# Kernel tuning notes

Measured on AMD Instinct MI355X. Metric: run time of the kernel, lower is better.

The kernel has to match this reference:

```python
import jax, jax.numpy as jnp
import numpy as np

SLOPE = 25.0          # snntorch surrogate.fast_sigmoid default slope
ALPHA = 0.05          # attenuation_alpha

@jax.custom_vjp
def spike_fn(x):
    return (x > 0).astype(x.dtype)

def _spike_fwd(x):
    return (x > 0).astype(x.dtype), x

def _spike_bwd(x, g):
    return (g / (SLOPE * jnp.abs(x) + 1.0) ** 2,)

spike_fn.defvjp(_spike_fwd, _spike_bwd)

def lstm_cell(x, h, c, W_ih, W_hh, b_ih, b_hh):
    gates = x @ W_ih.T + b_ih + h @ W_hh.T + b_hh  # [B, 4H]
    i, f, g, o = jnp.split(gates, 4, axis=-1)
    i = jax.nn.sigmoid(i); f = jax.nn.sigmoid(f)
    g = jnp.tanh(g);       o = jax.nn.sigmoid(o)
    c_new = f * c + i * g
    h_new = o * jnp.tanh(c_new)
    return h_new, c_new

def slstm_step(x, syn, mem, W_ih, W_hh, b_ih, b_hh, thr):
    # reset is detached in snntorch (mem_reset -> .detach())
    reset = jax.lax.stop_gradient((mem > thr).astype(mem.dtype))
    h, c = lstm_cell(x, mem, syn, W_ih, W_hh, b_ih, b_hh)
    mem_new = h - reset * thr          # subtract reset mechanism
    spk = spike_fn(mem_new - thr)      # surrogate-gradient spike
    return spk, c, mem_new

def setup_inputs() -> dict:
    key = jax.random.key(0)
    ks = jax.random.split(key, 12)
    T, B, I, H, C = 512, 256, 14, 512, 8
    s = 0.05
    return {
        "x":     jax.random.normal(ks[0], (T, B, I), jnp.float32),
        "W_ih1": jax.random.normal(ks[1], (4 * H, I), jnp.float32) * s,
        "W_hh1": jax.random.normal(ks[2], (4 * H, H), jnp.float32) * s,
        "b_ih1": jax.random.normal(ks[3], (4 * H,), jnp.float32) * s,
        "b_hh1": jax.random.normal(ks[4], (4 * H,), jnp.float32) * s,
        "thr1":  jnp.ones((), jnp.float32),
        "W_ih2": jax.random.normal(ks[5], (4 * H, H), jnp.float32) * s,
        "W_hh2": jax.random.normal(ks[6], (4 * H, H), jnp.float32) * s,
        "b_ih2": jax.random.normal(ks[7], (4 * H,), jnp.float32) * s,
        "b_hh2": jax.random.normal(ks[8], (4 * H,), jnp.float32) * s,
        "thr2":  jnp.ones((), jnp.float32),
        "W_fc":  jax.random.normal(ks[9], (C, H), jnp.float32) * s,
        "b_fc":  jax.random.normal(ks[10], (C,), jnp.float32) * s,
    }

def reference(x, W_ih1, W_hh1, b_ih1, b_hh1, thr1,
              W_ih2, W_hh2, b_ih2, b_hh2, thr2, W_fc, b_fc):
    T, B, _ = x.shape
    H = W_hh1.shape[1]
    zeros = jnp.zeros((B, H), x.dtype)
    init = (zeros, zeros, zeros, zeros)  # syn1, mem1, syn2, mem2

    def step(carry, xt):
        syn1, mem1, syn2, mem2 = carry
        spk1, syn1, mem1 = slstm_step(xt, syn1, mem1, W_ih1, W_hh1, b_ih1, b_hh1, thr1)
        spk2, syn2, mem2 = slstm_step(spk1, syn2, mem2, W_ih2, W_hh2, b_ih2, b_hh2, thr2)
        return (syn1, mem1, syn2, mem2), mem2

    _, mem2_rec = jax.lax.scan(step, init, x)  # [T, B, H]

    t_idx = jnp.arange(T, 0, -1, dtype=x.dtype)
    w = jnp.exp(-ALPHA * (t_idx - 1.0))
    w = w / w.sum()
    final_mem = jnp.einsum('tbh,t->bh', mem2_rec, w)
    return final_mem @ W_fc.T + b_fc
```

## Files before the change

kernel.cpp:

```cpp
#include <hip/hip_runtime.h>


typedef _Float16 half8 __attribute__((ext_vector_type(8)));
typedef float    floatx4 __attribute__((ext_vector_type(4)));
typedef int      int4v  __attribute__((ext_vector_type(4)));

union H8 { int4v i; half8 h; };

#define T_STEPS 512
#define HDIM    512
#define ROWS    32
#define HSLICE  16
#define ACT_ELEMS 16384
#define WS_ACT_OFF 4096
#define WS_PART_OFF (WS_ACT_OFF + 2*5*8*ACT_ELEMS*2)
#define WS_PART_BYTES (256*32*8*4)
#define WS_MEMSET_BYTES WS_PART_OFF
#define PB_STRIDE 17

__device__ __forceinline__ float sigm(float v)  { return 1.0f/(1.0f + __expf(-v)); }
__device__ __forceinline__ float tanhf_(float v){ return 1.0f - 2.0f/(__expf(2.0f*v) + 1.0f); }
__device__ __forceinline__ void split16(float v, _Float16& h, _Float16& l) {
  h = (_Float16)v; l = (_Float16)(v - (float)h);
}
__device__ __forceinline__ unsigned pack2(_Float16 a, _Float16 b) {
  unsigned short ua = __builtin_bit_cast(unsigned short, a);
  unsigned short ub = __builtin_bit_cast(unsigned short, b);
  return (unsigned)ua | ((unsigned)ub << 16);
}

#define LDG16(dst, ptr) \
  asm volatile("global_load_dwordx4 %0, %1, off sc0 sc1" : "=v"((dst).i) : "v"(ptr) : "memory")

__device__ __forceinline__ void st_u32(unsigned* p, unsigned v) {
  __hip_atomic_store(p, v, __ATOMIC_RELAXED, __HIP_MEMORY_SCOPE_AGENT);
}

#define MFMA(A,B,C) __builtin_amdgcn_mfma_f32_16x16x32_f16((A),(B),(C),0,0,0)

__global__ __launch_bounds__(256) __attribute__((amdgpu_waves_per_eu(1, 1)))
void slstm_kernel(const float* __restrict__ x,
                  const float* __restrict__ Wih1, const float* __restrict__ Whh1,
                  const float* __restrict__ bih1, const float* __restrict__ bhh1,
                  const float* __restrict__ thr1p,
                  const float* __restrict__ Wih2, const float* __restrict__ Whh2,
                  const float* __restrict__ bih2, const float* __restrict__ bhh2,
                  const float* __restrict__ thr2p,
                  const float* __restrict__ Wfc,  const float* __restrict__ bfc,
                  float* __restrict__ out, unsigned char* __restrict__ ws)
{
  const int tid  = threadIdx.x;
  const int bid  = blockIdx.x;
  const int g    = bid & 7;
  const int cs   = bid >> 3;
  const int wave = tid >> 6;
  const int lane = tid & 63;
  const int l15  = lane & 15;
  const int lg   = lane >> 4;
  const int kr   = lg*8;

  __shared__ _Float16 wIloLds[4*16*64*8];
  __shared__ float    pbuf[4][128*PB_STRIDE + 16];
  __shared__ _Float16 xstage[ROWS*32];
  __shared__ float    b2s[64];

  unsigned* cntp  = (unsigned*)ws + (size_t)g*16;
  _Float16* actb  = (_Float16*)(ws + WS_ACT_OFF);
  float*    partb = (float*)(ws + WS_PART_OFF);

  half8 wAh[4][4], wAl[4][4], wIh[4][4], wHh[4][4], wHl[4][4];
#pragma unroll
  for (int q = 0; q < 4; ++q) {
    const int gcq = q*HDIM + cs*HSLICE + l15;
#pragma unroll
    for (int kl = 0; kl < 4; ++kl) {
      const int kb = wave*4 + kl;
      const float* p1 = Whh1 + (size_t)gcq*HDIM + kb*32 + kr;
      const float* p2 = Wih2 + (size_t)gcq*HDIM + kb*32 + kr;
      const float* p3 = Whh2 + (size_t)gcq*HDIM + kb*32 + kr;
      half8 ah, al, ih, il, hh, hl;
#pragma unroll
      for (int j = 0; j < 8; ++j) {
        _Float16 sh, sl;
        split16(p1[j], sh, sl); ah[j] = sh; al[j] = sl;
        split16(p2[j], sh, sl); ih[j] = sh; il[j] = sl;
        split16(p3[j], sh, sl); hh[j] = sh; hl[j] = sl;
      }
      wAh[q][kl] = ah; wAl[q][kl] = al; wIh[q][kl] = ih;
      wHh[q][kl] = hh; wHl[q][kl] = hl;
      *(half8*)&wIloLds[(((wave*4 + kl)*4 + q)*64 + lane)*8] = il;
    }
  }
  half8 wX1, wX2;
  {
    const int gcx = wave*HDIM + cs*HSLICE + l15;
#pragma unroll
    for (int j = 0; j < 8; ++j) {
      int k = kr + j;
      float v1 = 0.0f, v2 = 0.0f;
      _Float16 h, l;
      if (k < 14)       { split16(Wih1[(size_t)gcx*14 + k], h, l); v1 = (float)h; v2 = (float)l; }
      else if (k == 14) { split16(bih1[gcx] + bhh1[gcx], h, l); v1 = (float)h; }
      else if (k == 15) { split16(bih1[gcx] + bhh1[gcx], h, l); v1 = (float)l; }
      else if (k <= 29) { split16(Wih1[(size_t)gcx*14 + (k - 16)], h, l); v2 = (float)h; }
      wX1[j] = (_Float16)v1; wX2[j] = (_Float16)v2;
    }
  }
  if (tid < 64) {
    int q = tid >> 4, h = tid & 15;
    int gcl = q*HDIM + cs*HSLICE + h;
    b2s[tid] = bih2[gcl] + bhh2[gcl];
  }
  for (int idx = tid; idx < ROWS*32; idx += 256) {
    int k = idx & 31;
    if (k == 14 || k == 15) xstage[idx] = (_Float16)1.0f;
    else if (k >= 30)       xstage[idx] = (_Float16)0.0f;
  }
  __syncthreads();

  const float thr1 = thr1p[0], thr2 = thr2p[0];
  const int eb  = tid >> 3;
  const int ehl = (tid & 7)*2;
  const int ehg = cs*HSLICE + ehl;
  const int g16 = ((ehg >> 5)*2 + (eb >> 4))*64 + ((ehg >> 3) & 3)*16 + (eb & 15);
  const int u32i = g16*4 + ((ehg & 7) >> 1);
  const int r0 = tid/14,  k0 = tid%14;
  const int i1 = tid + 256;
  const int r1 = i1/14,   k1 = i1%14;

  float syn1[2] = {0,0}, m1p[2] = {0,0}, syn2[2] = {0,0}, m2p[2] = {0,0};
  float accf[2] = {0,0};
  const float invn = (1.0f - __expf(-0.05f)) / (1.0f - __expf(-0.05f*512.0f));
  int bar_dead = 0;

  for (int t = 0; t < T_STEPS; ++t) {
    const int wp = t & 1, rp = wp ^ 1;

    const float* xt = x + ((size_t)t*256 + (size_t)g*ROWS)*14;
    { _Float16 h, l; split16(xt[r0*14 + k0], h, l);
      xstage[r0*32 + k0] = h; xstage[r0*32 + 16 + k0] = l; }
    if (i1 < 448) {
      _Float16 h, l; split16(xt[r1*14 + k1], h, l);
      xstage[r1*32 + k1] = h; xstage[r1*32 + 16 + k1] = l; }
    __syncthreads();

    const char* baseH = (const char*)(actb + (size_t)((rp*5 + 0)*8 + g)*ACT_ELEMS);
    const char* baseL = (const char*)(actb + (size_t)((rp*5 + 1)*8 + g)*ACT_ELEMS);
    H8 fh[4][2], fl[4][2];
#pragma unroll
    for (int kl = 0; kl < 4; ++kl) {
      const int kb = wave*4 + kl;
      const size_t o0 = (size_t)(((kb*2 + 0)*64 + lane)*16);
      const size_t o1 = (size_t)(((kb*2 + 1)*64 + lane)*16);
      LDG16(fh[kl][0], baseH + o0);  LDG16(fh[kl][1], baseH + o1);
      LDG16(fl[kl][0], baseL + o0);  LDG16(fl[kl][1], baseL + o1);
    }
    floatx4 acc[4][2];
#pragma unroll
    for (int q = 0; q < 4; ++q) { acc[q][0] = (floatx4){0,0,0,0}; acc[q][1] = (floatx4){0,0,0,0}; }
    {
      half8 xa0 = *(const half8*)&xstage[l15*32 + kr];
      half8 xa1 = *(const half8*)&xstage[(16 + l15)*32 + kr];
      acc[wave][0] = MFMA(xa0, wX1, acc[wave][0]);  acc[wave][1] = MFMA(xa1, wX1, acc[wave][1]);
      acc[wave][0] = MFMA(xa0, wX2, acc[wave][0]);  acc[wave][1] = MFMA(xa1, wX2, acc[wave][1]);
    }
    asm volatile("s_waitcnt vmcnt(8)"
      : "+v"(fh[0][0].i), "+v"(fh[0][1].i), "+v"(fl[0][0].i), "+v"(fl[0][1].i),
        "+v"(fh[1][0].i), "+v"(fh[1][1].i), "+v"(fl[1][0].i), "+v"(fl[1][1].i)
      : : "memory");
#pragma unroll
    for (int kl = 0; kl < 2; ++kl)
#pragma unroll
      for (int q = 0; q < 4; ++q) {
        acc[q][0] = MFMA(fh[kl][0].h, wAh[q][kl], acc[q][0]);
        acc[q][1] = MFMA(fh[kl][1].h, wAh[q][kl], acc[q][1]);
        acc[q][0] = MFMA(fh[kl][0].h, wAl[q][kl], acc[q][0]);
        acc[q][1] = MFMA(fh[kl][1].h, wAl[q][kl], acc[q][1]);
        acc[q][0] = MFMA(fl[kl][0].h, wAh[q][kl], acc[q][0]);
        acc[q][1] = MFMA(fl[kl][1].h, wAh[q][kl], acc[q][1]);
      }
    asm volatile("s_waitcnt vmcnt(0)"
      : "+v"(fh[2][0].i), "+v"(fh[2][1].i), "+v"(fl[2][0].i), "+v"(fl[2][1].i),
        "+v"(fh[3][0].i), "+v"(fh[3][1].i), "+v"(fl[3][0].i), "+v"(fl[3][1].i)
      : : "memory");
#pragma unroll
    for (int kl = 2; kl < 4; ++kl)
#pragma unroll
      for (int q = 0; q < 4; ++q) {
        acc[q][0] = MFMA(fh[kl][0].h, wAh[q][kl], acc[q][0]);
        acc[q][1] = MFMA(fh[kl][1].h, wAh[q][kl], acc[q][1]);
        acc[q][0] = MFMA(fh[kl][0].h, wAl[q][kl], acc[q][0]);
        acc[q][1] = MFMA(fh[kl][1].h, wAl[q][kl], acc[q][1]);
        acc[q][0] = MFMA(fl[kl][0].h, wAh[q][kl], acc[q][0]);
        acc[q][1] = MFMA(fl[kl][1].h, wAh[q][kl], acc[q][1]);
      }
#pragma unroll
    for (int q = 0; q < 4; ++q)
#pragma unroll
      for (int tl = 0; tl < 2; ++tl)
#pragma unroll
        for (int p = 0; p < 4; ++p)
          pbuf[wave][(q*32 + tl*16 + lg*4 + p)*PB_STRIDE + l15] = acc[q][tl][p];
    __syncthreads();

    {
      unsigned* m1hW = (unsigned*)(actb + (size_t)((wp*5 + 0)*8 + g)*ACT_ELEMS);
      unsigned* m1lW = (unsigned*)(actb + (size_t)((wp*5 + 1)*8 + g)*ACT_ELEMS);
      unsigned* spW  = (unsigned*)(actb + (size_t)((wp*5 + 2)*8 + g)*ACT_ELEMS);
      _Float16 mh[2], ml[2], sp[2];
#pragma unroll
      for (int c = 0; c < 2; ++c) {
        float pi = 0, pf = 0, pg = 0, po = 0;
#pragma unroll
        for (int w = 0; w < 4; ++w) {
          pi += pbuf[w][(0*32 + eb)*PB_STRIDE + ehl + c];
          pf += pbuf[w][(1*32 + eb)*PB_STRIDE + ehl + c];
          pg += pbuf[w][(2*32 + eb)*PB_STRIDE + ehl + c];
          po += pbuf[w][(3*32 + eb)*PB_STRIDE + ehl + c];
        }
        float iv = sigm(pi), fv = sigm(pf), gv = tanhf_(pg), ov = sigm(po);
        float cnew = fv*syn1[c] + iv*gv;
        syn1[c] = cnew;
        float hnew = ov*tanhf_(cnew);
        float m1 = hnew - ((m1p[c] > thr1) ? thr1 : 0.0f);
        m1p[c] = m1;
        split16(m1, mh[c], ml[c]);
        sp[c] = ((m1 - thr1) > 0.0f) ? (_Float16)1.0f : (_Float16)0.0f;
      }
      st_u32(m1hW + u32i, pack2(mh[0], mh[1]));
      st_u32(m1lW + u32i, pack2(ml[0], ml[1]));
      st_u32(spW  + u32i, pack2(sp[0], sp[1]));
    }

    asm volatile("s_waitcnt vmcnt(0)" ::: "memory");
    __syncthreads();
    if (tid == 0 && !bar_dead) {
      __hip_atomic_fetch_add(cntp, 1u, __ATOMIC_RELAXED, __HIP_MEMORY_SCOPE_AGENT);
      unsigned target = 32u*(unsigned)(t + 1);
      int tries = 0;
      while (__hip_atomic_load(cntp, __ATOMIC_RELAXED, __HIP_MEMORY_SCOPE_AGENT) < target) {
        __builtin_amdgcn_s_sleep(1);
        if (++tries > (1 << 20)) { bar_dead = 1; break; }
      }
    }
    __syncthreads();
    __atomic_signal_fence(__ATOMIC_SEQ_CST);

    const char* baseS  = (const char*)(actb + (size_t)((wp*5 + 2)*8 + g)*ACT_ELEMS);
    const char* base2H = (const char*)(actb + (size_t)((rp*5 + 3)*8 + g)*ACT_ELEMS);
    const char* base2L = (const char*)(actb + (size_t)((rp*5 + 4)*8 + g)*ACT_ELEMS);
#pragma unroll
    for (int q = 0; q < 4; ++q) { acc[q][0] = (floatx4){0,0,0,0}; acc[q][1] = (floatx4){0,0,0,0}; }
#pragma unroll
    for (int hc = 0; hc < 2; ++hc) {
      H8 sb[2][2], mbh[2][2], mbl[2][2];
#pragma unroll
      for (int kc = 0; kc < 2; ++kc) {
        const int kb = wave*4 + hc*2 + kc;
        const size_t o0 = (size_t)(((kb*2 + 0)*64 + lane)*16);
        const size_t o1 = (size_t)(((kb*2 + 1)*64 + lane)*16);
        LDG16(sb[kc][0],  baseS  + o0);  LDG16(sb[kc][1],  baseS  + o1);
        LDG16(mbh[kc][0], base2H + o0);  LDG16(mbh[kc][1], base2H + o1);
        LDG16(mbl[kc][0], base2L + o0);  LDG16(mbl[kc][1], base2L + o1);
      }
      asm volatile("s_waitcnt vmcnt(0)"
        : "+v"(sb[0][0].i), "+v"(sb[0][1].i), "+v"(mbh[0][0].i), "+v"(mbh[0][1].i),
          "+v"(mbl[0][0].i), "+v"(mbl[0][1].i),
          "+v"(sb[1][0].i), "+v"(sb[1][1].i), "+v"(mbh[1][0].i), "+v"(mbh[1][1].i),
          "+v"(mbl[1][0].i), "+v"(mbl[1][1].i)
        : : "memory");
#pragma unroll
      for (int kc = 0; kc < 2; ++kc) {
        const int kl = hc*2 + kc;
#pragma unroll
        for (int q = 0; q < 4; ++q) {
          half8 wIl = *(const half8*)&wIloLds[(((wave*4 + kl)*4 + q)*64 + lane)*8];
          acc[q][0] = MFMA(sb[kc][0].h,  wIh[q][kl], acc[q][0]);
          acc[q][1] = MFMA(sb[kc][1].h,  wIh[q][kl], acc[q][1]);
          acc[q][0] = MFMA(sb[kc][0].h,  wIl,        acc[q][0]);
          acc[q][1] = MFMA(sb[kc][1].h,  wIl,        acc[q][1]);
          acc[q][0] = MFMA(mbh[kc][0].h, wHh[q][kl], acc[q][0]);
          acc[q][1] = MFMA(mbh[kc][1].h, wHh[q][kl], acc[q][1]);
          acc[q][0] = MFMA(mbh[kc][0].h, wHl[q][kl], acc[q][0]);
          acc[q][1] = MFMA(mbh[kc][1].h, wHl[q][kl], acc[q][1]);
          acc[q][0] = MFMA(mbl[kc][0].h, wHh[q][kl], acc[q][0]);
          acc[q][1] = MFMA(mbl[kc][1].h, wHh[q][kl], acc[q][1]);
        }
      }
    }
#pragma unroll
    for (int q = 0; q < 4; ++q)
#pragma unroll
      for (int tl = 0; tl < 2; ++tl)
#pragma unroll
        for (int p = 0; p < 4; ++p)
          pbuf[wave][(q*32 + tl*16 + lg*4 + p)*PB_STRIDE + l15] = acc[q][tl][p];
    __syncthreads();

    float wt = __expf(0.05f*(float)(t + 1 - T_STEPS)) * invn;
    {
      unsigned* m2hW = (unsigned*)(actb + (size_t)((wp*5 + 3)*8 + g)*ACT_ELEMS);
      unsigned* m2lW = (unsigned*)(actb + (size_t)((wp*5 + 4)*8 + g)*ACT_ELEMS);
      _Float16 mh[2], ml[2];
#pragma unroll
      for (int c = 0; c < 2; ++c) {
        float pi = b2s[0*16 + ehl + c], pf = b2s[1*16 + ehl + c];
        float pg = b2s[2*16 + ehl + c], po = b2s[3*16 + ehl + c];
#pragma unroll
        for (int w = 0; w < 4; ++w) {
          pi += pbuf[w][(0*32 + eb)*PB_STRIDE + ehl + c];
          pf += pbuf[w][(1*32 + eb)*PB_STRIDE + ehl + c];
          pg += pbuf[w][(2*32 + eb)*PB_STRIDE + ehl + c];
          po += pbuf[w][(3*32 + eb)*PB_STRIDE + ehl + c];
        }
        float iv = sigm(pi), fv = sigm(pf), gv = tanhf_(pg), ov = sigm(po);
        float cnew = fv*syn2[c] + iv*gv;
        syn2[c] = cnew;
        float hnew = ov*tanhf_(cnew);
        float m2 = hnew - ((m2p[c] > thr2) ? thr2 : 0.0f);
        m2p[c] = m2;
        accf[c] += wt * m2;
        split16(m2, mh[c], ml[c]);
      }
      st_u32(m2hW + u32i, pack2(mh[0], mh[1]));
      st_u32(m2lW + u32i, pack2(ml[0], ml[1]));
    }
  }

  float part[8];
#pragma unroll
  for (int c = 0; c < 8; ++c)
    part[c] = accf[0]*Wfc[c*HDIM + ehg] + accf[1]*Wfc[c*HDIM + ehg + 1];
#pragma unroll
  for (int off = 1; off < 8; off <<= 1)
#pragma unroll
    for (int c = 0; c < 8; ++c)
      part[c] += __shfl_xor(part[c], off, 64);
  {
    int c = tid & 7;
    __hip_atomic_store(&partb[((size_t)(g*32 + cs)*32 + (size_t)eb)*8 + c], part[c],
                       __ATOMIC_RELAXED, __HIP_MEMORY_SCOPE_AGENT);
  }
  asm volatile("s_waitcnt vmcnt(0)" ::: "memory");
  __syncthreads();
  if (tid == 0 && !bar_dead) {
    __hip_atomic_fetch_add(cntp, 1u, __ATOMIC_RELAXED, __HIP_MEMORY_SCOPE_AGENT);
    unsigned target = 32u*513u;
    int tries = 0;
    while (__hip_atomic_load(cntp, __ATOMIC_RELAXED, __HIP_MEMORY_SCOPE_AGENT) < target) {
      __builtin_amdgcn_s_sleep(1);
      if (++tries > (1 << 20)) break;
    }
  }
  __syncthreads();
  __atomic_signal_fence(__ATOMIC_SEQ_CST);

  if (cs == 0) {
    int b = tid >> 3, c = tid & 7;
    float s = bfc[c];
#pragma unroll 4
    for (int jj = 0; jj < 32; ++jj)
      s += __hip_atomic_load(&partb[((size_t)(g*32 + jj)*32 + (size_t)b)*8 + c],
                             __ATOMIC_RELAXED, __HIP_MEMORY_SCOPE_AGENT);
    out[(g*ROWS + b)*8 + c] = s;
  }
}

extern "C" void kernel_launch(void* const* d_in, const int* in_sizes, int n_in,
                              void* d_out, int out_size, void* d_ws, size_t ws_size,
                              hipStream_t stream) {
  (void)in_sizes; (void)n_in;
  const float* x    = (const float*)d_in[0];
  const float* Wih1 = (const float*)d_in[1];
  const float* Whh1 = (const float*)d_in[2];
  const float* bih1 = (const float*)d_in[3];
  const float* bhh1 = (const float*)d_in[4];
  const float* thr1 = (const float*)d_in[5];
  const float* Wih2 = (const float*)d_in[6];
  const float* Whh2 = (const float*)d_in[7];
  const float* bih2 = (const float*)d_in[8];
  const float* bhh2 = (const float*)d_in[9];
  const float* thr2 = (const float*)d_in[10];
  const float* Wfc  = (const float*)d_in[11];
  const float* bfc  = (const float*)d_in[12];
  float* out = (float*)d_out;
  unsigned char* ws = (unsigned char*)d_ws;

  if (ws_size < (size_t)(WS_PART_OFF + WS_PART_BYTES)) {
    hipError_t e1 = hipMemsetAsync(d_out, 0x7f, (size_t)out_size*4, stream);
    (void)e1;
    return;
  }
  hipError_t e2 = hipMemsetAsync(d_ws, 0, WS_MEMSET_BYTES, stream);
  (void)e2;

  slstm_kernel<<<dim3(256), dim3(256), 0, stream>>>(
      x, Wih1, Whh1, bih1, bhh1, thr1,
      Wih2, Whh2, bih2, bhh2, thr2, Wfc, bfc, out, ws);
}
```

Measured before the change: 4.821 ms.

## Prefetch next step's layer-1 state during layer-2 phase and vectorize partial reductions

The loads of the next timestep's layer-1 membrane (hi/lo fp16 halves) move out of the top of the loop and are issued during the layer-2 phase, right after that step's grid barrier makes them visible. Their latency then overlaps with the layer-2 MFMA work. The layer-2 loads are also split into two halves so the second batch is in flight during the first half's MFMAs. Cross-wave partial-sum reads from LDS become float2 vector loads, with the stride padded to 18 for alignment. This keeps more registers live across the loop and relies on the memory ordering of the prefetch relative to the barrier.

```diff
diff --git a/kernel.cpp b/kernel.cpp
--- a/kernel.cpp
+++ b/kernel.cpp
@@ -3,6 +3,7 @@
 
 typedef _Float16 half8 __attribute__((ext_vector_type(8)));
 typedef float    floatx4 __attribute__((ext_vector_type(4)));
+typedef float    float2v __attribute__((ext_vector_type(2)));
 typedef int      int4v  __attribute__((ext_vector_type(4)));
 
 union H8 { int4v i; half8 h; };
@@ -16,7 +17,7 @@
 #define WS_PART_OFF (WS_ACT_OFF + 2*5*8*ACT_ELEMS*2)
 #define WS_PART_BYTES (256*32*8*4)
 #define WS_MEMSET_BYTES WS_PART_OFF
-#define PB_STRIDE 17
+#define PB_STRIDE 18
 
 __device__ __forceinline__ float sigm(float v)  { return 1.0f/(1.0f + __expf(-v)); }
 __device__ __forceinline__ float tanhf_(float v){ return 1.0f - 2.0f/(__expf(2.0f*v) + 1.0f); }
@@ -133,6 +134,25 @@
   const float invn = (1.0f - __expf(-0.05f)) / (1.0f - __expf(-0.05f*512.0f));
   int bar_dead = 0;
 
+  size_t oA[4][2];
+#pragma unroll
+  for (int kl = 0; kl < 4; ++kl) {
+    const int kb = wave*4 + kl;
+    oA[kl][0] = (size_t)(((kb*2 + 0)*64 + lane)*16);
+    oA[kl][1] = (size_t)(((kb*2 + 1)*64 + lane)*16);
+  }
+
+  H8 fh[4][2], fl[4][2];
+  {
+    const char* pH = (const char*)(actb + (size_t)((1*5 + 0)*8 + g)*ACT_ELEMS);
+    const char* pL = (const char*)(actb + (size_t)((1*5 + 1)*8 + g)*ACT_ELEMS);
+#pragma unroll
+    for (int kl = 0; kl < 4; ++kl) {
+      LDG16(fh[kl][0], pH + oA[kl][0]);  LDG16(fh[kl][1], pH + oA[kl][1]);
+      LDG16(fl[kl][0], pL + oA[kl][0]);  LDG16(fl[kl][1], pL + oA[kl][1]);
+    }
+  }
+
   for (int t = 0; t < T_STEPS; ++t) {
     const int wp = t & 1, rp = wp ^ 1;
 
@@ -144,17 +164,6 @@
       xstage[r1*32 + k1] = h; xstage[r1*32 + 16 + k1] = l; }
     __syncthreads();
 
-    const char* baseH = (const char*)(actb + (size_t)((rp*5 + 0)*8 + g)*ACT_ELEMS);
-    const char* baseL = (const char*)(actb + (size_t)((rp*5 + 1)*8 + g)*ACT_ELEMS);
-    H8 fh[4][2], fl[4][2];
-#pragma unroll
-    for (int kl = 0; kl < 4; ++kl) {
-      const int kb = wave*4 + kl;
-      const size_t o0 = (size_t)(((kb*2 + 0)*64 + lane)*16);
-      const size_t o1 = (size_t)(((kb*2 + 1)*64 + lane)*16);
-      LDG16(fh[kl][0], baseH + o0);  LDG16(fh[kl][1], baseH + o1);
-      LDG16(fl[kl][0], baseL + o0);  LDG16(fl[kl][1], baseL + o1);
-    }
     floatx4 acc[4][2];
 #pragma unroll
     for (int q = 0; q < 4; ++q) { acc[q][0] = (floatx4){0,0,0,0}; acc[q][1] = (floatx4){0,0,0,0}; }
@@ -164,12 +173,14 @@
       acc[wave][0] = MFMA(xa0, wX1, acc[wave][0]);  acc[wave][1] = MFMA(xa1, wX1, acc[wave][1]);
       acc[wave][0] = MFMA(xa0, wX2, acc[wave][0]);  acc[wave][1] = MFMA(xa1, wX2, acc[wave][1]);
     }
-    asm volatile("s_waitcnt vmcnt(8)"
+    asm volatile("s_waitcnt vmcnt(0)"
       : "+v"(fh[0][0].i), "+v"(fh[0][1].i), "+v"(fl[0][0].i), "+v"(fl[0][1].i),
-        "+v"(fh[1][0].i), "+v"(fh[1][1].i), "+v"(fl[1][0].i), "+v"(fl[1][1].i)
+        "+v"(fh[1][0].i), "+v"(fh[1][1].i), "+v"(fl[1][0].i), "+v"(fl[1][1].i),
+        "+v"(fh[2][0].i), "+v"(fh[2][1].i), "+v"(fl[2][0].i), "+v"(fl[2][1].i),
+        "+v"(fh[3][0].i), "+v"(fh[3][1].i), "+v"(fl[3][0].i), "+v"(fl[3][1].i)
       : : "memory");
 #pragma unroll
-    for (int kl = 0; kl < 2; ++kl)
+    for (int kl = 0; kl < 4; ++kl)
 #pragma unroll
       for (int q = 0; q < 4; ++q) {
         acc[q][0] = MFMA(fh[kl][0].h, wAh[q][kl], acc[q][0]);
@@ -179,21 +190,6 @@
         acc[q][0] = MFMA(fl[kl][0].h, wAh[q][kl], acc[q][0]);
         acc[q][1] = MFMA(fl[kl][1].h, wAh[q][kl], acc[q][1]);
       }
-    asm volatile("s_waitcnt vmcnt(0)"
-      : "+v"(fh[2][0].i), "+v"(fh[2][1].i), "+v"(fl[2][0].i), "+v"(fl[2][1].i),
-        "+v"(fh[3][0].i), "+v"(fh[3][1].i), "+v"(fl[3][0].i), "+v"(fl[3][1].i)
-      : : "memory");
-#pragma unroll
-    for (int kl = 2; kl < 4; ++kl)
-#pragma unroll
-      for (int q = 0; q < 4; ++q) {
-        acc[q][0] = MFMA(fh[kl][0].h, wAh[q][kl], acc[q][0]);
-        acc[q][1] = MFMA(fh[kl][1].h, wAh[q][kl], acc[q][1]);
-        acc[q][0] = MFMA(fh[kl][0].h, wAl[q][kl], acc[q][0]);
-        acc[q][1] = MFMA(fh[kl][1].h, wAl[q][kl], acc[q][1]);
-        acc[q][0] = MFMA(fl[kl][0].h, wAh[q][kl], acc[q][0]);
-        acc[q][1] = MFMA(fl[kl][1].h, wAh[q][kl], acc[q][1]);
-      }
 #pragma unroll
     for (int q = 0; q < 4; ++q)
 #pragma unroll
@@ -207,18 +203,18 @@
       unsigned* m1hW = (unsigned*)(actb + (size_t)((wp*5 + 0)*8 + g)*ACT_ELEMS);
       unsigned* m1lW = (unsigned*)(actb + (size_t)((wp*5 + 1)*8 + g)*ACT_ELEMS);
       unsigned* spW  = (unsigned*)(actb + (size_t)((wp*5 + 2)*8 + g)*ACT_ELEMS);
+      float2v pi2 = {0,0}, pf2 = {0,0}, pg2 = {0,0}, po2 = {0,0};
+#pragma unroll
+      for (int w = 0; w < 4; ++w) {
+        pi2 += *(const float2v*)&pbuf[w][(0*32 + eb)*PB_STRIDE + ehl];
+        pf2 += *(const float2v*)&pbuf[w][(1*32 + eb)*PB_STRIDE + ehl];
+        pg2 += *(const float2v*)&pbuf[w][(2*32 + eb)*PB_STRIDE + ehl];
+        po2 += *(const float2v*)&pbuf[w][(3*32 + eb)*PB_STRIDE + ehl];
+      }
       _Float16 mh[2], ml[2], sp[2];
 #pragma unroll
       for (int c = 0; c < 2; ++c) {
-        float pi = 0, pf = 0, pg = 0, po = 0;
-#pragma unroll
-        for (int w = 0; w < 4; ++w) {
-          pi += pbuf[w][(0*32 + eb)*PB_STRIDE + ehl + c];
-          pf += pbuf[w][(1*32 + eb)*PB_STRIDE + ehl + c];
-          pg += pbuf[w][(2*32 + eb)*PB_STRIDE + ehl + c];
-          po += pbuf[w][(3*32 + eb)*PB_STRIDE + ehl + c];
-        }
-        float iv = sigm(pi), fv = sigm(pf), gv = tanhf_(pg), ov = sigm(po);
+        float iv = sigm(pi2[c]), fv = sigm(pf2[c]), gv = tanhf_(pg2[c]), ov = sigm(po2[c]);
         float cnew = fv*syn1[c] + iv*gv;
         syn1[c] = cnew;
         float hnew = ov*tanhf_(cnew);
@@ -249,43 +245,75 @@
     const char* baseS  = (const char*)(actb + (size_t)((wp*5 + 2)*8 + g)*ACT_ELEMS);
     const char* base2H = (const char*)(actb + (size_t)((rp*5 + 3)*8 + g)*ACT_ELEMS);
     const char* base2L = (const char*)(actb + (size_t)((rp*5 + 4)*8 + g)*ACT_ELEMS);
+    const char* nH = (const char*)(actb + (size_t)((wp*5 + 0)*8 + g)*ACT_ELEMS);
+    const char* nL = (const char*)(actb + (size_t)((wp*5 + 1)*8 + g)*ACT_ELEMS);
 #pragma unroll
     for (int q = 0; q < 4; ++q) { acc[q][0] = (floatx4){0,0,0,0}; acc[q][1] = (floatx4){0,0,0,0}; }
-#pragma unroll
-    for (int hc = 0; hc < 2; ++hc) {
-      H8 sb[2][2], mbh[2][2], mbl[2][2];
-#pragma unroll
-      for (int kc = 0; kc < 2; ++kc) {
-        const int kb = wave*4 + hc*2 + kc;
-        const size_t o0 = (size_t)(((kb*2 + 0)*64 + lane)*16);
-        const size_t o1 = (size_t)(((kb*2 + 1)*64 + lane)*16);
-        LDG16(sb[kc][0],  baseS  + o0);  LDG16(sb[kc][1],  baseS  + o1);
-        LDG16(mbh[kc][0], base2H + o0);  LDG16(mbh[kc][1], base2H + o1);
-        LDG16(mbl[kc][0], base2L + o0);  LDG16(mbl[kc][1], base2L + o1);
-      }
-      asm volatile("s_waitcnt vmcnt(0)"
-        : "+v"(sb[0][0].i), "+v"(sb[0][1].i), "+v"(mbh[0][0].i), "+v"(mbh[0][1].i),
-          "+v"(mbl[0][0].i), "+v"(mbl[0][1].i),
-          "+v"(sb[1][0].i), "+v"(sb[1][1].i), "+v"(mbh[1][0].i), "+v"(mbh[1][1].i),
-          "+v"(mbl[1][0].i), "+v"(mbl[1][1].i)
-        : : "memory");
-#pragma unroll
-      for (int kc = 0; kc < 2; ++kc) {
-        const int kl = hc*2 + kc;
-#pragma unroll
-        for (int q = 0; q < 4; ++q) {
-          half8 wIl = *(const half8*)&wIloLds[(((wave*4 + kl)*4 + q)*64 + lane)*8];
-          acc[q][0] = MFMA(sb[kc][0].h,  wIh[q][kl], acc[q][0]);
-          acc[q][1] = MFMA(sb[kc][1].h,  wIh[q][kl], acc[q][1]);
-          acc[q][0] = MFMA(sb[kc][0].h,  wIl,        acc[q][0]);
-          acc[q][1] = MFMA(sb[kc][1].h,  wIl,        acc[q][1]);
-          acc[q][0] = MFMA(mbh[kc][0].h, wHh[q][kl], acc[q][0]);
-          acc[q][1] = MFMA(mbh[kc][1].h, wHh[q][kl], acc[q][1]);
-          acc[q][0] = MFMA(mbh[kc][0].h, wHl[q][kl], acc[q][0]);
-          acc[q][1] = MFMA(mbh[kc][1].h, wHl[q][kl], acc[q][1]);
-          acc[q][0] = MFMA(mbl[kc][0].h, wHh[q][kl], acc[q][0]);
-          acc[q][1] = MFMA(mbl[kc][1].h, wHh[q][kl], acc[q][1]);
-        }
+
+    H8 sb[2][2], mbh[2][2], mbl[2][2];
+#pragma unroll
+    for (int kc = 0; kc < 2; ++kc) {
+      LDG16(sb[kc][0],  baseS  + oA[kc][0]);  LDG16(sb[kc][1],  baseS  + oA[kc][1]);
+      LDG16(mbh[kc][0], base2H + oA[kc][0]);  LDG16(mbh[kc][1], base2H + oA[kc][1]);
+      LDG16(mbl[kc][0], base2L + oA[kc][0]);  LDG16(mbl[kc][1], base2L + oA[kc][1]);
+    }
+    asm volatile("s_waitcnt vmcnt(0)"
+      : "+v"(sb[0][0].i), "+v"(sb[0][1].i), "+v"(mbh[0][0].i), "+v"(mbh[0][1].i),
+        "+v"(mbl[0][0].i), "+v"(mbl[0][1].i),
+        "+v"(sb[1][0].i), "+v"(sb[1][1].i), "+v"(mbh[1][0].i), "+v"(mbh[1][1].i),
+        "+v"(mbl[1][0].i), "+v"(mbl[1][1].i)
+      : : "memory");
+#pragma unroll
+    for (int kc = 0; kc < 2; ++kc) {
+      const int kl = kc;
+#pragma unroll
+      for (int q = 0; q < 4; ++q) {
+        half8 wIl = *(const half8*)&wIloLds[(((wave*4 + kl)*4 + q)*64 + lane)*8];
+        acc[q][0] = MFMA(sb[kc][0].h,  wIh[q][kl], acc[q][0]);
+        acc[q][1] = MFMA(sb[kc][1].h,  wIh[q][kl], acc[q][1]);
+        acc[q][0] = MFMA(sb[kc][0].h,  wIl,        acc[q][0]);
+        acc[q][1] = MFMA(sb[kc][1].h,  wIl,        acc[q][1]);
+        acc[q][0] = MFMA(mbh[kc][0].h, wHh[q][kl], acc[q][0]);
+        acc[q][1] = MFMA(mbh[kc][1].h, wHh[q][kl], acc[q][1]);
+        acc[q][0] = MFMA(mbh[kc][0].h, wHl[q][kl], acc[q][0]);
+        acc[q][1] = MFMA(mbh[kc][1].h, wHl[q][kl], acc[q][1]);
+        acc[q][0] = MFMA(mbl[kc][0].h, wHh[q][kl], acc[q][0]);
+        acc[q][1] = MFMA(mbl[kc][1].h, wHh[q][kl], acc[q][1]);
+      }
+    }
+#pragma unroll
+    for (int kc = 0; kc < 2; ++kc) {
+      LDG16(sb[kc][0],  baseS  + oA[2+kc][0]);  LDG16(sb[kc][1],  baseS  + oA[2+kc][1]);
+      LDG16(mbh[kc][0], base2H + oA[2+kc][0]);  LDG16(mbh[kc][1], base2H + oA[2+kc][1]);
+      LDG16(mbl[kc][0], base2L + oA[2+kc][0]);  LDG16(mbl[kc][1], base2L + oA[2+kc][1]);
+    }
+#pragma unroll
+    for (int kl = 0; kl < 4; ++kl) {
+      LDG16(fh[kl][0], nH + oA[kl][0]);  LDG16(fh[kl][1], nH + oA[kl][1]);
+      LDG16(fl[kl][0], nL + oA[kl][0]);  LDG16(fl[kl][1], nL + oA[kl][1]);
+    }
+    asm volatile("s_waitcnt vmcnt(16)"
+      : "+v"(sb[0][0].i), "+v"(sb[0][1].i), "+v"(mbh[0][0].i), "+v"(mbh[0][1].i),
+        "+v"(mbl[0][0].i), "+v"(mbl[0][1].i),
+        "+v"(sb[1][0].i), "+v"(sb[1][1].i), "+v"(mbh[1][0].i), "+v"(mbh[1][1].i),
+        "+v"(mbl[1][0].i), "+v"(mbl[1][1].i)
+      : : "memory");
+#pragma unroll
+    for (int kc = 0; kc < 2; ++kc) {
+      const int kl = 2 + kc;
+#pragma unroll
+      for (int q = 0; q < 4; ++q) {
+        half8 wIl = *(const half8*)&wIloLds[(((wave*4 + kl)*4 + q)*64 + lane)*8];
+        acc[q][0] = MFMA(sb[kc][0].h,  wIh[q][kl], acc[q][0]);
+        acc[q][1] = MFMA(sb[kc][1].h,  wIh[q][kl], acc[q][1]);
+        acc[q][0] = MFMA(sb[kc][0].h,  wIl,        acc[q][0]);
+        acc[q][1] = MFMA(sb[kc][1].h,  wIl,        acc[q][1]);
+        acc[q][0] = MFMA(mbh[kc][0].h, wHh[q][kl], acc[q][0]);
+        acc[q][1] = MFMA(mbh[kc][1].h, wHh[q][kl], acc[q][1]);
+        acc[q][0] = MFMA(mbh[kc][0].h, wHl[q][kl], acc[q][0]);
+        acc[q][1] = MFMA(mbh[kc][1].h, wHl[q][kl], acc[q][1]);
+        acc[q][0] = MFMA(mbl[kc][0].h, wHh[q][kl], acc[q][0]);
+        acc[q][1] = MFMA(mbl[kc][1].h, wHh[q][kl], acc[q][1]);
       }
     }
 #pragma unroll
@@ -301,19 +329,22 @@
     {
       unsigned* m2hW = (unsigned*)(actb + (size_t)((wp*5 + 3)*8 + g)*ACT_ELEMS);
       unsigned* m2lW = (unsigned*)(actb + (size_t)((wp*5 + 4)*8 + g)*ACT_ELEMS);
+      float2v pi2, pf2, pg2, po2;
+      pi2 = *(const float2v*)&b2s[0*16 + ehl];
+      pf2 = *(const float2v*)&b2s[1*16 + ehl];
+      pg2 = *(const float2v*)&b2s[2*16 + ehl];
+      po2 = *(const float2v*)&b2s[3*16 + ehl];
+#pragma unroll
+      for (int w = 0; w < 4; ++w) {
+        pi2 += *(const float2v*)&pbuf[w][(0*32 + eb)*PB_STRIDE + ehl];
+        pf2 += *(const float2v*)&pbuf[w][(1*32 + eb)*PB_STRIDE + ehl];
+        pg2 += *(const float2v*)&pbuf[w][(2*32 + eb)*PB_STRIDE + ehl];
+        po2 += *(const float2v*)&pbuf[w][(3*32 + eb)*PB_STRIDE + ehl];
+      }
       _Float16 mh[2], ml[2];
 #pragma unroll
       for (int c = 0; c < 2; ++c) {
-        float pi = b2s[0*16 + ehl + c], pf = b2s[1*16 + ehl + c];
-        float pg = b2s[2*16 + ehl + c], po = b2s[3*16 + ehl + c];
-#pragma unroll
-        for (int w = 0; w < 4; ++w) {
-          pi += pbuf[w][(0*32 + eb)*PB_STRIDE + ehl + c];
-          pf += pbuf[w][(1*32 + eb)*PB_STRIDE + ehl + c];
-          pg += pbuf[w][(2*32 + eb)*PB_STRIDE + ehl + c];
-          po += pbuf[w][(3*32 + eb)*PB_STRIDE + ehl + c];
-        }
-        float iv = sigm(pi), fv = sigm(pf), gv = tanhf_(pg), ov = sigm(po);
+        float iv = sigm(pi2[c]), fv = sigm(pf2[c]), gv = tanhf_(pg2[c]), ov = sigm(po2[c]);
         float cnew = fv*syn2[c] + iv*gv;
         syn2[c] = cnew;
         float hnew = ov*tanhf_(cnew);
```

After: 4.855 ms. Within noise of the previous version (+0.7%).
